# Optimization experiments

Measured on AMD Instinct MI355X. Metric: run time of the kernel, lower is better.

Reference implementation:

```python
import jax, jax.numpy as jnp
import numpy as np

K = 5  # spline kernel size per dim (dim=3 -> 125 kernels)
NS = [20000, 5000, 1280, 320, 80, 32, 16]
ES = [320000, 80000, 20480, 5120, 1280, 512]
NF = [2, 16, 32, 64, 128, 128, 128]

_BITS = jnp.array([[(b >> d) & 1 for d in range(3)] for b in range(8)], dtype=jnp.int32)  # [8,3]
_STRIDES = jnp.array([1, K, K * K], dtype=jnp.int32)


def spline_conv(x, edge_index, pseudo, W, root, bias):
    """SplineConv, dim=3, kernel_size=5, degree-1 open B-splines, mean aggregation.
    x: [N,Cin], edge_index: [2,E], pseudo: [E,3] in [0,1], W: [125,Cin,Cout]."""
    N, Cin = x.shape
    src, dst = edge_index[0], edge_index[1]
    p = pseudo * (K - 1)                                  # [E,3]
    k0 = jnp.clip(jnp.floor(p), 0.0, K - 2)
    frac = p - k0                                         # [E,3]
    k0 = k0.astype(jnp.int32)
    # degree-1 basis: 2^3 = 8 active kernel corners per edge
    w = jnp.where(_BITS[None] == 1, frac[:, None, :], 1.0 - frac[:, None, :])  # [E,8,3]
    wprod = jnp.prod(w, axis=-1)                          # [E,8]
    kidx = jnp.sum((k0[:, None, :] + _BITS[None]) * _STRIDES, axis=-1)         # [E,8]
    xj = x[src]                                           # gather [E,Cin]
    # scatter weighted source features into (dst node, kernel) buckets
    seg = (dst[:, None] * (K ** 3) + kidx).reshape(-1)    # [E*8]
    contrib = (wprod[..., None] * xj[:, None, :]).reshape(-1, Cin)
    A = jax.ops.segment_sum(contrib, seg, num_segments=N * K ** 3).reshape(N, K ** 3, Cin)
    out = jnp.einsum('nki,kio->no', A, W)                 # [N,Cout]
    deg = jax.ops.segment_sum(jnp.ones(src.shape[0], x.dtype), dst, num_segments=N)
    out = out / jnp.maximum(deg, 1.0)[:, None]            # mean aggregation
    return out + x @ root + bias                          # root weight + bias


def _forward(x, eis, eas, Ps, Ws, Rs, bs):
    for l in range(6):
        h = jax.nn.elu(spline_conv(x, eis[l], eas[l], Ws[l], Rs[l], bs[l]))
        x = Ps[l].T @ h                                   # pool to coarser mesh
    return jnp.max(x, axis=0)[None, :]                    # AdaptiveMaxPool1d(1) over nodes -> [1,128]


def setup_inputs() -> dict:
    key = jax.random.key(0)
    ks = iter(jax.random.split(key, 64))
    inp = {"x": jax.random.normal(next(ks), (NS[0], NF[0]), jnp.float32)}
    for l in range(6):
        inp[f"ei{l}"] = jax.random.randint(next(ks), (2, ES[l]), 0, NS[l], dtype=jnp.int32)
        inp[f"ea{l}"] = jax.random.uniform(next(ks), (ES[l], 3), jnp.float32)
    pnames = ["P01", "P12", "P23", "P34", "P45", "P56"]
    for l, pn in enumerate(pnames):
        inp[pn] = jax.random.normal(next(ks), (NS[l], NS[l + 1]), jnp.float32) * (NS[l] ** -0.5)
    for l in range(6):
        cin, cout = NF[l], NF[l + 1]
        inp[f"W{l+1}"] = jax.random.normal(next(ks), (K ** 3, cin, cout), jnp.float32) * 0.05
        inp[f"R{l+1}"] = jax.random.normal(next(ks), (cin, cout), jnp.float32) * (cin ** -0.5)
        inp[f"b{l+1}"] = jnp.zeros((cout,), jnp.float32)
    return inp


def reference(x, ei0, ea0, ei1, ea1, ei2, ea2, ei3, ea3, ei4, ea4, ei5, ea5,
              P01, P12, P23, P34, P45, P56,
              W1, R1, b1, W2, R2, b2, W3, R3, b3,
              W4, R4, b4, W5, R5, b5, W6, R6, b6):
    eis = [ei0, ei1, ei2, ei3, ei4, ei5]
    eas = [ea0, ea1, ea2, ea3, ea4, ea5]
    Ps = [P01, P12, P23, P34, P45, P56]
    Ws = [W1, W2, W3, W4, W5, W6]
    Rs = [R1, R2, R3, R4, R5, R6]
    bs = [b1, b2, b3, b4, b5, b6]
    return _forward(x, eis, eas, Ps, Ws, Rs, bs)
```

## Files before the change

### kernel.cpp

```cpp
#include <hip/hip_runtime.h>
#include <math.h>

#define NKER 125

struct Ptr6i { const int* p[6]; };
struct Ptr6f { const float* p[6]; };

__global__ __launch_bounds__(256) void hist_all_kernel(Ptr6i eis, int* __restrict__ hist) {
  static const int EB[7] = {0, 1250, 1563, 1643, 1663, 1668, 1670};
  static const int Es[6] = {320000, 80000, 20480, 5120, 1280, 512};
  static const int hOff[6] = {0, 20000, 25000, 26280, 26600, 26680};
  int b = blockIdx.x;
  int l = 0;
  while (b >= EB[l + 1]) l++;
  int e = (b - EB[l]) * 256 + threadIdx.x;
  if (e < Es[l]) atomicAdd(&hist[hOff[l] + eis.p[l][Es[l] + e]], 1);
}

__global__ __launch_bounds__(1024) void scan6_kernel(int* __restrict__ hist,
                                                     int* __restrict__ start,
                                                     int* __restrict__ cursor) {
  static const int histOff[6] = {0, 20000, 25000, 26280, 26600, 26680};
  static const int startOff[6] = {0, 20001, 25002, 26283, 26604, 26685};
  static const int Nl[6] = {20000, 5000, 1280, 320, 80, 32};
  __shared__ int ps[1024];
  int b = blockIdx.x;
  int* h = hist + histOff[b];
  int* s = start + startOff[b];
  int* c = cursor + histOff[b];
  int N = Nl[b];
  int t = threadIdx.x;
  int chunk = (N + 1023) / 1024;
  int lo = min(N, t * chunk), hi = min(N, lo + chunk);
  int sum = 0;
  for (int i = lo; i < hi; i++) sum += h[i];
  ps[t] = sum;
  __syncthreads();
  for (int off = 1; off < 1024; off <<= 1) {
    int v = (t >= off) ? ps[t - off] : 0;
    __syncthreads();
    ps[t] += v;
    __syncthreads();
  }
  int base = (t == 0) ? 0 : ps[t - 1];
  for (int i = lo; i < hi; i++) {
    int hv = h[i];
    s[i] = base;
    c[i] = base;
    base += hv;
  }
  if (t == 1023) s[N] = ps[1023];
}

__global__ __launch_bounds__(256) void reorder_all_kernel(
    Ptr6i eis, Ptr6f eas, int* __restrict__ cursor,
    int* __restrict__ srcS, int* __restrict__ kpkS, float* __restrict__ frS) {
  static const int EB[7] = {0, 1250, 1563, 1643, 1663, 1668, 1670};
  static const int Es[6] = {320000, 80000, 20480, 5120, 1280, 512};
  static const int hOff[6] = {0, 20000, 25000, 26280, 26600, 26680};
  static const int EoffK[6] = {0, 320000, 400000, 420480, 425600, 426880};
  int b = blockIdx.x;
  int l = 0;
  while (b >= EB[l + 1]) l++;
  int e = (b - EB[l]) * 256 + threadIdx.x;
  if (e >= Es[l]) return;
  const int* ei = eis.p[l];
  const float* ea = eas.p[l];
  int src = ei[e];
  int dst = ei[Es[l] + e];
  int kpk = 0;
  float f[3];
#pragma unroll
  for (int d = 0; d < 3; d++) {
    float p = ea[e * 3 + d] * 4.0f;
    float kf = fminf(fmaxf(floorf(p), 0.0f), 3.0f);
    f[d] = p - kf;
    kpk |= ((int)kf) << (4 * d);
  }
  int pos = EoffK[l] + atomicAdd(&cursor[hOff[l] + dst], 1);
  srcS[pos] = src;
  kpkS[pos] = kpk;
  frS[pos * 3 + 0] = f[0];
  frS[pos * 3 + 1] = f[1];
  frS[pos * 3 + 2] = f[2];
}

template <int CINSH, int G, int KDIM, int KSG, int NT>
__global__ __launch_bounds__(NT) void build2_kernel(
    const int* __restrict__ start, const int* __restrict__ srcS,
    const int* __restrict__ kpkS, const float* __restrict__ frS,
    const float* __restrict__ x, float* __restrict__ A) {
  __shared__ float rows[G * KDIM];
  const int Cin = 1 << CINSH;
  int tid = threadIdx.x;
  int n0 = blockIdx.x * G;
  for (int t = tid; t < G * KDIM / 4; t += NT)
    ((float4*)rows)[t] = make_float4(0.0f, 0.0f, 0.0f, 0.0f);
  __syncthreads();
  int nl = tid >> CINSH;
  int ci = tid & (Cin - 1);
  int n = n0 + nl;
  int e0 = start[n], e1 = start[n + 1];
  float* row = rows + nl * KDIM + ci;
  for (int e = e0; e < e1; e++) {
    int src = srcS[e];
    int kpk = kpkS[e];
    float f0 = frS[3 * e], f1 = frS[3 * e + 1], f2 = frS[3 * e + 2];
    float xv = x[((size_t)src << CINSH) + ci];
    float g0 = 1.0f - f0, g1 = 1.0f - f1, g2 = 1.0f - f2;
    int kb = (kpk & 15) + 5 * ((kpk >> 4) & 15) + 25 * ((kpk >> 8) & 15);
    float* rb = row + (kb << CINSH);
    rb[0]              += (g0 * g1 * g2) * xv;
    rb[1 << CINSH]     += (f0 * g1 * g2) * xv;
    rb[5 << CINSH]     += (g0 * f1 * g2) * xv;
    rb[6 << CINSH]     += (f0 * f1 * g2) * xv;
    rb[25 << CINSH]    += (g0 * g1 * f2) * xv;
    rb[26 << CINSH]    += (f0 * g1 * f2) * xv;
    rb[30 << CINSH]    += (g0 * f1 * f2) * xv;
    rb[31 << CINSH]    += (f0 * f1 * f2) * xv;
  }
  __syncthreads();
  const int RQ = KSG / 4;
  for (int t = tid; t < G * RQ; t += NT) {
    int r = t / RQ, c4 = t % RQ;
    int c = c4 * 4;
    float4 v = make_float4(0.0f, 0.0f, 0.0f, 0.0f);
    if (c < KDIM) v = *(const float4*)&rows[r * KDIM + c];
    ((float4*)&A[(size_t)(n0 + r) * KSG])[c4] = v;
  }
}

__global__ __launch_bounds__(128) void build2_l0_kernel(
    const int* __restrict__ start, const int* __restrict__ srcS,
    const int* __restrict__ kpkS, const float* __restrict__ frS,
    const float* __restrict__ x, float* __restrict__ A, int N) {
  __shared__ float rows[64 * 254];
  int tid = threadIdx.x;
  int n0 = blockIdx.x * 64;
  for (int t = tid; t < 64 * 254 / 4; t += 128)
    ((float4*)rows)[t] = make_float4(0.0f, 0.0f, 0.0f, 0.0f);
  __syncthreads();
  int nl = tid >> 1;
  int ci = tid & 1;
  int n = n0 + nl;
  if (n < N) {
    int e0 = start[n], e1 = start[n + 1];
    float* row = rows + nl * 254 + ci;
    for (int e = e0; e < e1; e++) {
      int src = srcS[e];
      int kpk = kpkS[e];
      float f0 = frS[3 * e], f1 = frS[3 * e + 1], f2 = frS[3 * e + 2];
      float xv = x[(size_t)src * 2 + ci];
      float g0 = 1.0f - f0, g1 = 1.0f - f1, g2 = 1.0f - f2;
      int kb = (kpk & 15) + 5 * ((kpk >> 4) & 15) + 25 * ((kpk >> 8) & 15);
      float* rb = row + kb * 2;
      rb[0]  = fmaf(g0 * g1 * g2, xv, rb[0]);
      rb[2]  = fmaf(f0 * g1 * g2, xv, rb[2]);
      rb[10] = fmaf(g0 * f1 * g2, xv, rb[10]);
      rb[12] = fmaf(f0 * f1 * g2, xv, rb[12]);
      rb[50] = fmaf(g0 * g1 * f2, xv, rb[50]);
      rb[52] = fmaf(f0 * g1 * f2, xv, rb[52]);
      rb[60] = fmaf(g0 * f1 * f2, xv, rb[60]);
      rb[62] = fmaf(f0 * f1 * f2, xv, rb[62]);
    }
  }
  __syncthreads();
  for (int it = 0; it < 32; it++) {
    int sub = tid >> 6;
    int c4 = tid & 63;
    int nn = n0 + it * 2 + sub;
    if (nn >= N) continue;
    float4 v = make_float4(0.0f, 0.0f, 0.0f, 0.0f);
    if (c4 < 63) v = *(const float4*)&rows[(it * 2 + sub) * 254 + c4 * 4];
    ((float4*)&A[(size_t)nn * 256])[c4] = v;
  }
}

template <int BM, int COUT, int NT>
__global__ __launch_bounds__(NT) void gemm3_kernel(
    const float* __restrict__ A, const float* __restrict__ W,
    float* __restrict__ gpart, int M, int Kdim, int KS, int ktiles) {
  const int BK = 32;
  __shared__ float At[BK][BM + 4];
  __shared__ float Wl[BK][COUT];
  const int TC = COUT / 4;
  int tid = threadIdx.x;
  int tc = tid % TC;
  int tr = tid / TC;
  int m0 = blockIdx.x * BM;
  int kbeg = blockIdx.y * ktiles * BK;
  int kend = min(KS, kbeg + ktiles * BK);
  float ar[4][4];
#pragma unroll
  for (int i = 0; i < 4; i++)
#pragma unroll
    for (int j = 0; j < 4; j++) ar[i][j] = 0.0f;

  for (int k0 = kbeg; k0 < kend; k0 += BK) {
    for (int t = tid; t < BM * (BK / 4); t += NT) {
      int c4 = t % (BK / 4), r = t / (BK / 4);
      int m = m0 + r;
      float4 v = make_float4(0.0f, 0.0f, 0.0f, 0.0f);
      if (m < M) v = *(const float4*)&A[(size_t)m * KS + k0 + c4 * 4];
      At[c4 * 4 + 0][r] = v.x; At[c4 * 4 + 1][r] = v.y;
      At[c4 * 4 + 2][r] = v.z; At[c4 * 4 + 3][r] = v.w;
    }
    int kleft = Kdim - k0;
    if (kleft >= BK) {
      for (int t = tid; t < BK * COUT / 4; t += NT)
        ((float4*)&Wl[0][0])[t] = ((const float4*)&W[(size_t)k0 * COUT])[t];
    } else {
      for (int t = tid; t < BK * COUT; t += NT) {
        int kk = t / COUT, o = t % COUT;
        Wl[kk][o] = (kk < kleft) ? W[(size_t)(k0 + kk) * COUT + o] : 0.0f;
      }
    }
    __syncthreads();
#pragma unroll
    for (int kk = 0; kk < BK; kk++) {
      float4 a = *(const float4*)&At[kk][tr * 4];
      float4 w = *(const float4*)&Wl[kk][tc * 4];
      float av[4] = {a.x, a.y, a.z, a.w};
      float wv[4] = {w.x, w.y, w.z, w.w};
#pragma unroll
      for (int i = 0; i < 4; i++)
#pragma unroll
        for (int j = 0; j < 4; j++)
          ar[i][j] = fmaf(av[i], wv[j], ar[i][j]);
    }
    __syncthreads();
  }
  float* gp = gpart + ((size_t)blockIdx.y * M) * COUT + tc * 4;
#pragma unroll
  for (int i = 0; i < 4; i++) {
    int m = m0 + tr * 4 + i;
    if (m < M)
      *(float4*)(gp + (size_t)m * COUT) =
          make_float4(ar[i][0], ar[i][1], ar[i][2], ar[i][3]);
  }
}

__global__ __launch_bounds__(256) void epilogue_kernel(
    const float* __restrict__ gpart, const int* __restrict__ degI,
    const float* __restrict__ x, const float* __restrict__ R,
    const float* __restrict__ b, float* __restrict__ h,
    int N, int Cin, int coutShift, int kchunks) {
  int tid = blockIdx.x * 256 + threadIdx.x;
  int Cout = 1 << coutShift;
  if (tid >= (N << coutShift)) return;
  int n = tid >> coutShift;
  int o = tid & (Cout - 1);
  size_t stride = (size_t)N << coutShift;
  float s = 0.0f;
  for (int c = 0; c < kchunks; c++) s += gpart[(size_t)c * stride + tid];
  s /= (float)max(degI[n], 1);
  float r = b[o];
  const float* xr = &x[n * Cin];
  for (int i = 0; i < Cin; i++) r = fmaf(xr[i], R[i * Cout + o], r);
  float v = s + r;
  h[tid] = v > 0.0f ? v : expm1f(v);
}

#define FMA4(c, pj, h) \
  c.x = fmaf(pj, h.x, c.x); c.y = fmaf(pj, h.y, c.y); \
  c.z = fmaf(pj, h.z, c.z); c.w = fmaf(pj, h.w, c.w);

template <int COUT, int OPT>
__global__ __launch_bounds__(256) void pool5b_kernel(
    const float* __restrict__ P, const float* __restrict__ h,
    float* __restrict__ partial, int Nsrc, int Nnext, int chunk, int items) {
  extern __shared__ float hs[];
  int c = blockIdx.y;
  int n0 = c * chunk;
  int n1 = min(Nsrc, n0 + chunk);
  int len = n1 - n0;
  for (int t = threadIdx.x; t < len * (COUT / 4); t += 256)
    ((float4*)hs)[t] = ((const float4*)&h[(size_t)n0 * COUT])[t];
  __syncthreads();
  int item = blockIdx.x * 256 + threadIdx.x;
  if (item >= items) return;
  int nj4 = Nnext >> 2;
  int j0 = (item % nj4) << 2;
  int o0 = (item / nj4) * OPT;
  const float4 z = make_float4(0.0f, 0.0f, 0.0f, 0.0f);
  float4 c00 = z, c01 = z, c02 = z, c03 = z;
  float4 c10 = z, c11 = z, c12 = z, c13 = z;
  float4 c20 = z, c21 = z, c22 = z, c23 = z;
  float4 c30 = z, c31 = z, c32 = z, c33 = z;
  const float* Pb = P + j0;

#define USTEP(pv, nn)                                                    \
  {                                                                      \
    const float4* hr = (const float4*)&hs[(nn) * COUT + o0];             \
    float4 h0 = hr[0], h1 = hr[1];                                       \
    FMA4(c00, pv.x, h0) FMA4(c01, pv.x, h1)                              \
    FMA4(c10, pv.y, h0) FMA4(c11, pv.y, h1)                              \
    FMA4(c20, pv.z, h0) FMA4(c21, pv.z, h1)                              \
    FMA4(c30, pv.w, h0) FMA4(c31, pv.w, h1)                              \
    if constexpr (OPT == 16) {                                           \
      float4 h2 = hr[2], h3 = hr[3];                                     \
      FMA4(c02, pv.x, h2) FMA4(c03, pv.x, h3)                            \
      FMA4(c12, pv.y, h2) FMA4(c13, pv.y, h3)                            \
      FMA4(c22, pv.z, h2) FMA4(c23, pv.z, h3)                            \
      FMA4(c32, pv.w, h2) FMA4(c33, pv.w, h3)                            \
    }                                                                    \
  }

  int n = 0;
  for (; n + 4 <= len; n += 4) {
    float4 pv0 = *(const float4*)&Pb[(size_t)(n0 + n + 0) * Nnext];
    float4 pv1 = *(const float4*)&Pb[(size_t)(n0 + n + 1) * Nnext];
    float4 pv2 = *(const float4*)&Pb[(size_t)(n0 + n + 2) * Nnext];
    float4 pv3 = *(const float4*)&Pb[(size_t)(n0 + n + 3) * Nnext];
    USTEP(pv0, n + 0)
    USTEP(pv1, n + 1)
    USTEP(pv2, n + 2)
    USTEP(pv3, n + 3)
  }
  for (; n < len; n++) {
    float4 pv = *(const float4*)&Pb[(size_t)(n0 + n) * Nnext];
    USTEP(pv, n)
  }
#undef USTEP

  float* pp = partial + ((size_t)c * Nnext + j0) * COUT + o0;
  *(float4*)(pp + 0 * COUT + 0) = c00;
  *(float4*)(pp + 0 * COUT + 4) = c01;
  *(float4*)(pp + 1 * COUT + 0) = c10;
  *(float4*)(pp + 1 * COUT + 4) = c11;
  *(float4*)(pp + 2 * COUT + 0) = c20;
  *(float4*)(pp + 2 * COUT + 4) = c21;
  *(float4*)(pp + 3 * COUT + 0) = c30;
  *(float4*)(pp + 3 * COUT + 4) = c31;
  if constexpr (OPT == 16) {
    *(float4*)(pp + 0 * COUT + 8)  = c02;
    *(float4*)(pp + 0 * COUT + 12) = c03;
    *(float4*)(pp + 1 * COUT + 8)  = c12;
    *(float4*)(pp + 1 * COUT + 12) = c13;
    *(float4*)(pp + 2 * COUT + 8)  = c22;
    *(float4*)(pp + 2 * COUT + 12) = c23;
    *(float4*)(pp + 3 * COUT + 8)  = c32;
    *(float4*)(pp + 3 * COUT + 12) = c33;
  }
}

__global__ __launch_bounds__(256) void preduce_kernel(
    const float* __restrict__ partial, float* __restrict__ xnext,
    int NnCout, int chunks) {
  int i = blockIdx.x * 256 + threadIdx.x;
  if (i >= NnCout) return;
  float s = 0.0f;
  for (int c = 0; c < chunks; c++) s += partial[(size_t)c * NnCout + i];
  xnext[i] = s;
}

__global__ __launch_bounds__(128) void max_kernel(const float* __restrict__ x6,
                                                  float* __restrict__ out) {
  int o = threadIdx.x;
  float m = -3.0e38f;
  for (int n = 0; n < 16; n++) m = fmaxf(m, x6[n * 128 + o]);
  out[o] = m;
}

extern "C" void kernel_launch(void* const* d_in, const int* in_sizes, int n_in,
                              void* d_out, int out_size, void* d_ws, size_t ws_size,
                              hipStream_t stream) {
  static const int NSh[7] = {20000, 5000, 1280, 320, 80, 32, 16};
  static const int ESh[6] = {320000, 80000, 20480, 5120, 1280, 512};
  static const int NFh[7] = {2, 16, 32, 64, 128, 128, 128};
  static const int cinSh[6]  = {1, 4, 5, 6, 7, 7};
  static const int coutSh[6] = {4, 5, 6, 7, 7, 7};
  static const int KSt[6] = {256, 2016, 4000, 8000, 16000, 16000};
  static const int kchunksTab[6] = {4, 8, 16, 32, 64, 128};
  static const int ktilesTab[6]  = {2, 8, 8, 8, 8, 4};
  static const int poolChunksTab[6] = {250, 80, 16, 8, 4, 2};
  static const int histOff[6] = {0, 20000, 25000, 26280, 26600, 26680};
  static const int startOff[6] = {0, 20001, 25002, 26283, 26604, 26685};
  static const int Eoff[6] = {0, 320000, 400000, 420480, 425600, 426880};

  const float* x0 = (const float*)d_in[0];
  Ptr6i eis;
  Ptr6f eas;
  for (int l = 0; l < 6; l++) {
    eis.p[l] = (const int*)d_in[1 + 2 * l];
    eas.p[l] = (const float*)d_in[2 + 2 * l];
  }
  const float* Pm[6];
  for (int l = 0; l < 6; l++) Pm[l] = (const float*)d_in[13 + l];
  const float* Wt[6];
  const float* Rt[6];
  const float* bt[6];
  for (int l = 0; l < 6; l++) {
    Wt[l] = (const float*)d_in[19 + 3 * l];
    Rt[l] = (const float*)d_in[20 + 3 * l];
    bt[l] = (const float*)d_in[21 + 3 * l];
  }

  float* ws = (float*)d_ws;
  float* A     = ws;
  float* gpart = ws + 10150000;
  float* hbuf  = ws + 11500000;
  float* ppart = ws + 12000000;
  float* xA    = ws + 32100000;
  float* xB    = ws + 32200000;
  int* hist    = (int*)(ws + 32300000);
  int* startA  = (int*)(ws + 32330000);
  int* cursor  = (int*)(ws + 32360000);
  int* srcS    = (int*)(ws + 32390000);
  int* kpkS    = (int*)(ws + 32900000);
  float* frS   = ws + 33400000;

  hipMemsetAsync(hist, 0, 26712 * sizeof(int), stream);
  hist_all_kernel<<<1670, 256, 0, stream>>>(eis, hist);
  scan6_kernel<<<6, 1024, 0, stream>>>(hist, startA, cursor);
  reorder_all_kernel<<<1670, 256, 0, stream>>>(eis, eas, cursor, srcS, kpkS, frS);

  const float* cur = x0;
  for (int l = 0; l < 6; l++) {
    int N = NSh[l], Nn = NSh[l + 1], Cin = NFh[l], Cout = NFh[l + 1];
    int Kdim = NKER * Cin, KS = KSt[l];
    float* xnext = (l & 1) ? xB : xA;
    const int* st = startA + startOff[l];
    const int* ss = srcS + Eoff[l];
    const int* kk = kpkS + Eoff[l];
    const float* ff = frS + 3 * (size_t)Eoff[l];

    switch (l) {
      case 0: build2_l0_kernel<<<313, 128, 0, stream>>>(st, ss, kk, ff, cur, A, N); break;
      case 1: build2_kernel<4, 8, 2000, 2016, 128><<<625, 128, 0, stream>>>(st, ss, kk, ff, cur, A); break;
      case 2: build2_kernel<5, 4, 4000, 4000, 128><<<320, 128, 0, stream>>>(st, ss, kk, ff, cur, A); break;
      case 3: build2_kernel<6, 2, 8000, 8000, 128><<<160, 128, 0, stream>>>(st, ss, kk, ff, cur, A); break;
      case 4: build2_kernel<7, 1, 16000, 16000, 128><<<80, 128, 0, stream>>>(st, ss, kk, ff, cur, A); break;
      default: build2_kernel<7, 1, 16000, 16000, 128><<<32, 128, 0, stream>>>(st, ss, kk, ff, cur, A); break;
    }

    int kchunks = kchunksTab[l], ktiles = ktilesTab[l];
    switch (l) {
      case 0: {
        dim3 g((N + 127) / 128, kchunks);
        gemm3_kernel<128, 16, 128><<<g, 128, 0, stream>>>(A, Wt[l], gpart, N, Kdim, KS, ktiles);
        break;
      }
      case 1: {
        dim3 g((N + 127) / 128, kchunks);
        gemm3_kernel<128, 32, 256><<<g, 256, 0, stream>>>(A, Wt[l], gpart, N, Kdim, KS, ktiles);
        break;
      }
      case 2: {
        dim3 g((N + 63) / 64, kchunks);
        gemm3_kernel<64, 64, 256><<<g, 256, 0, stream>>>(A, Wt[l], gpart, N, Kdim, KS, ktiles);
        break;
      }
      default: {
        dim3 g((N + 31) / 32, kchunks);
        gemm3_kernel<32, 128, 256><<<g, 256, 0, stream>>>(A, Wt[l], gpart, N, Kdim, KS, ktiles);
        break;
      }
    }

    int ethreads = N << coutSh[l];
    epilogue_kernel<<<(ethreads + 255) / 256, 256, 0, stream>>>(
        gpart, hist + histOff[l], cur, Rt[l], bt[l], hbuf, N, Cin, coutSh[l], kchunks);

    int pc = poolChunksTab[l];
    int chunk = (N + pc - 1) / pc;
    size_t ldsB = (size_t)chunk * Cout * sizeof(float);
    int items, gx;
    switch (Cout) {
      case 16:
        items = (Nn >> 2) * 1;
        gx = (items + 255) / 256;
        pool5b_kernel<16, 16><<<dim3(gx, pc), 256, ldsB, stream>>>(Pm[l], hbuf, ppart, N, Nn, chunk, items);
        break;
      case 32:
        items = (Nn >> 2) * 2;
        gx = (items + 255) / 256;
        pool5b_kernel<32, 16><<<dim3(gx, pc), 256, ldsB, stream>>>(Pm[l], hbuf, ppart, N, Nn, chunk, items);
        break;
      case 64:
        items = (Nn >> 2) * 8;
        gx = (items + 255) / 256;
        pool5b_kernel<64, 8><<<dim3(gx, pc), 256, ldsB, stream>>>(Pm[l], hbuf, ppart, N, Nn, chunk, items);
        break;
      default:
        items = (Nn >> 2) * 16;
        gx = (items + 255) / 256;
        pool5b_kernel<128, 8><<<dim3(gx, pc), 256, ldsB, stream>>>(Pm[l], hbuf, ppart, N, Nn, chunk, items);
        break;
    }
    int NnCout = Nn << coutSh[l];
    preduce_kernel<<<(NnCout + 255) / 256, 256, 0, stream>>>(ppart, xnext, NnCout, pc);

    cur = xnext;
  }

  max_kernel<<<1, 128, 0, stream>>>(cur, (float*)d_out);
}
```

Measured before the change: 823.4 us.

## Pack sorted edge records into float4 and precompute atomic ranks during histogram

The histogram pass now records each edge's atomic rank within its destination bucket, so the placement pass computes its position from the scanned start offsets instead of doing a second round of atomics on a cursor array. Each sorted edge is stored as one float4 record, with src and the packed kernel index bit-packed into the first word and the three fractions in the rest. This lets the build kernels fetch an edge with one 16-byte load instead of five scalar loads. The pooling chunk count for layer 0 is also lowered. The bit packing relies on src fitting in 15 bits, which holds for node counts up to 32768.

Measured after the change: 755.1 us. -8.3%, faster.

```diff
diff --git a/kernel.cpp b/kernel.cpp
--- a/kernel.cpp
+++ b/kernel.cpp
@@ -6,28 +6,31 @@
 struct Ptr6i { const int* p[6]; };
 struct Ptr6f { const float* p[6]; };
 
-__global__ __launch_bounds__(256) void hist_all_kernel(Ptr6i eis, int* __restrict__ hist) {
+__global__ __launch_bounds__(256) void rank_all_kernel(Ptr6i eis, int* __restrict__ cnt,
+                                                       int* __restrict__ rankS) {
   static const int EB[7] = {0, 1250, 1563, 1643, 1663, 1668, 1670};
   static const int Es[6] = {320000, 80000, 20480, 5120, 1280, 512};
   static const int hOff[6] = {0, 20000, 25000, 26280, 26600, 26680};
+  static const int EoffK[6] = {0, 320000, 400000, 420480, 425600, 426880};
   int b = blockIdx.x;
   int l = 0;
   while (b >= EB[l + 1]) l++;
   int e = (b - EB[l]) * 256 + threadIdx.x;
-  if (e < Es[l]) atomicAdd(&hist[hOff[l] + eis.p[l][Es[l] + e]], 1);
-}
-
-__global__ __launch_bounds__(1024) void scan6_kernel(int* __restrict__ hist,
-                                                     int* __restrict__ start,
-                                                     int* __restrict__ cursor) {
+  if (e >= Es[l]) return;
+  int dst = eis.p[l][Es[l] + e];
+  int r = atomicAdd(&cnt[hOff[l] + dst], 1);
+  rankS[EoffK[l] + e] = r;
+}
+
+__global__ __launch_bounds__(1024) void scan6_kernel(const int* __restrict__ hist,
+                                                     int* __restrict__ start) {
   static const int histOff[6] = {0, 20000, 25000, 26280, 26600, 26680};
   static const int startOff[6] = {0, 20001, 25002, 26283, 26604, 26685};
   static const int Nl[6] = {20000, 5000, 1280, 320, 80, 32};
   __shared__ int ps[1024];
   int b = blockIdx.x;
-  int* h = hist + histOff[b];
+  const int* h = hist + histOff[b];
   int* s = start + startOff[b];
-  int* c = cursor + histOff[b];
   int N = Nl[b];
   int t = threadIdx.x;
   int chunk = (N + 1023) / 1024;
@@ -44,20 +47,18 @@
   }
   int base = (t == 0) ? 0 : ps[t - 1];
   for (int i = lo; i < hi; i++) {
-    int hv = h[i];
     s[i] = base;
-    c[i] = base;
-    base += hv;
+    base += h[i];
   }
   if (t == 1023) s[N] = ps[1023];
 }
 
-__global__ __launch_bounds__(256) void reorder_all_kernel(
-    Ptr6i eis, Ptr6f eas, int* __restrict__ cursor,
-    int* __restrict__ srcS, int* __restrict__ kpkS, float* __restrict__ frS) {
+__global__ __launch_bounds__(256) void place_all_kernel(
+    Ptr6i eis, Ptr6f eas, const int* __restrict__ startA,
+    const int* __restrict__ rankS, float4* __restrict__ recS) {
   static const int EB[7] = {0, 1250, 1563, 1643, 1663, 1668, 1670};
   static const int Es[6] = {320000, 80000, 20480, 5120, 1280, 512};
-  static const int hOff[6] = {0, 20000, 25000, 26280, 26600, 26680};
+  static const int sOff[6] = {0, 20001, 25002, 26283, 26604, 26685};
   static const int EoffK[6] = {0, 320000, 400000, 420480, 425600, 426880};
   int b = blockIdx.x;
   int l = 0;
@@ -77,18 +78,14 @@
     f[d] = p - kf;
     kpk |= ((int)kf) << (4 * d);
   }
-  int pos = EoffK[l] + atomicAdd(&cursor[hOff[l] + dst], 1);
-  srcS[pos] = src;
-  kpkS[pos] = kpk;
-  frS[pos * 3 + 0] = f[0];
-  frS[pos * 3 + 1] = f[1];
-  frS[pos * 3 + 2] = f[2];
+  int pos = startA[sOff[l] + dst] + rankS[EoffK[l] + e];
+  recS[EoffK[l] + pos] =
+      make_float4(__uint_as_float((unsigned)src | ((unsigned)kpk << 15)), f[0], f[1], f[2]);
 }
 
 template <int CINSH, int G, int KDIM, int KSG, int NT>
-__global__ __launch_bounds__(NT) void build2_kernel(
-    const int* __restrict__ start, const int* __restrict__ srcS,
-    const int* __restrict__ kpkS, const float* __restrict__ frS,
+__global__ __launch_bounds__(NT) void build3_kernel(
+    const int* __restrict__ start, const float4* __restrict__ recS,
     const float* __restrict__ x, float* __restrict__ A) {
   __shared__ float rows[G * KDIM];
   const int Cin = 1 << CINSH;
@@ -103,9 +100,11 @@
   int e0 = start[n], e1 = start[n + 1];
   float* row = rows + nl * KDIM + ci;
   for (int e = e0; e < e1; e++) {
-    int src = srcS[e];
-    int kpk = kpkS[e];
-    float f0 = frS[3 * e], f1 = frS[3 * e + 1], f2 = frS[3 * e + 2];
+    float4 rec = recS[e];
+    unsigned v = __float_as_uint(rec.x);
+    int src = v & 0x7fff;
+    int kpk = v >> 15;
+    float f0 = rec.y, f1 = rec.z, f2 = rec.w;
     float xv = x[((size_t)src << CINSH) + ci];
     float g0 = 1.0f - f0, g1 = 1.0f - f1, g2 = 1.0f - f2;
     int kb = (kpk & 15) + 5 * ((kpk >> 4) & 15) + 25 * ((kpk >> 8) & 15);
@@ -130,9 +129,8 @@
   }
 }
 
-__global__ __launch_bounds__(128) void build2_l0_kernel(
-    const int* __restrict__ start, const int* __restrict__ srcS,
-    const int* __restrict__ kpkS, const float* __restrict__ frS,
+__global__ __launch_bounds__(128) void build3_l0_kernel(
+    const int* __restrict__ start, const float4* __restrict__ recS,
     const float* __restrict__ x, float* __restrict__ A, int N) {
   __shared__ float rows[64 * 254];
   int tid = threadIdx.x;
@@ -147,9 +145,11 @@
     int e0 = start[n], e1 = start[n + 1];
     float* row = rows + nl * 254 + ci;
     for (int e = e0; e < e1; e++) {
-      int src = srcS[e];
-      int kpk = kpkS[e];
-      float f0 = frS[3 * e], f1 = frS[3 * e + 1], f2 = frS[3 * e + 2];
+      float4 rec = recS[e];
+      unsigned v = __float_as_uint(rec.x);
+      int src = v & 0x7fff;
+      int kpk = v >> 15;
+      float f0 = rec.y, f1 = rec.z, f2 = rec.w;
       float xv = x[(size_t)src * 2 + ci];
       float g0 = 1.0f - f0, g1 = 1.0f - f1, g2 = 1.0f - f2;
       int kb = (kpk & 15) + 5 * ((kpk >> 4) & 15) + 25 * ((kpk >> 8) & 15);
@@ -366,14 +366,13 @@
                               void* d_out, int out_size, void* d_ws, size_t ws_size,
                               hipStream_t stream) {
   static const int NSh[7] = {20000, 5000, 1280, 320, 80, 32, 16};
-  static const int ESh[6] = {320000, 80000, 20480, 5120, 1280, 512};
   static const int NFh[7] = {2, 16, 32, 64, 128, 128, 128};
   static const int cinSh[6]  = {1, 4, 5, 6, 7, 7};
   static const int coutSh[6] = {4, 5, 6, 7, 7, 7};
   static const int KSt[6] = {256, 2016, 4000, 8000, 16000, 16000};
   static const int kchunksTab[6] = {4, 8, 16, 32, 64, 128};
   static const int ktilesTab[6]  = {2, 8, 8, 8, 8, 4};
-  static const int poolChunksTab[6] = {250, 80, 16, 8, 4, 2};
+  static const int poolChunksTab[6] = {120, 80, 16, 8, 4, 2};
   static const int histOff[6] = {0, 20000, 25000, 26280, 26600, 26680};
   static const int startOff[6] = {0, 20001, 25002, 26283, 26604, 26685};
   static const int Eoff[6] = {0, 320000, 400000, 420480, 425600, 426880};
@@ -405,15 +404,13 @@
   float* xB    = ws + 32200000;
   int* hist    = (int*)(ws + 32300000);
   int* startA  = (int*)(ws + 32330000);
-  int* cursor  = (int*)(ws + 32360000);
-  int* srcS    = (int*)(ws + 32390000);
-  int* kpkS    = (int*)(ws + 32900000);
-  float* frS   = ws + 33400000;
+  int* rankS   = (int*)(ws + 32390000);
+  float4* recS = (float4*)(ws + 33000000);
 
   hipMemsetAsync(hist, 0, 26712 * sizeof(int), stream);
-  hist_all_kernel<<<1670, 256, 0, stream>>>(eis, hist);
-  scan6_kernel<<<6, 1024, 0, stream>>>(hist, startA, cursor);
-  reorder_all_kernel<<<1670, 256, 0, stream>>>(eis, eas, cursor, srcS, kpkS, frS);
+  rank_all_kernel<<<1670, 256, 0, stream>>>(eis, hist, rankS);
+  scan6_kernel<<<6, 1024, 0, stream>>>(hist, startA);
+  place_all_kernel<<<1670, 256, 0, stream>>>(eis, eas, startA, rankS, recS);
 
   const float* cur = x0;
   for (int l = 0; l < 6; l++) {
@@ -421,17 +418,15 @@
     int Kdim = NKER * Cin, KS = KSt[l];
     float* xnext = (l & 1) ? xB : xA;
     const int* st = startA + startOff[l];
-    const int* ss = srcS + Eoff[l];
-    const int* kk = kpkS + Eoff[l];
-    const float* ff = frS + 3 * (size_t)Eoff[l];
+    const float4* rc = recS + Eoff[l];
 
     switch (l) {
-      case 0: build2_l0_kernel<<<313, 128, 0, stream>>>(st, ss, kk, ff, cur, A, N); break;
-      case 1: build2_kernel<4, 8, 2000, 2016, 128><<<625, 128, 0, stream>>>(st, ss, kk, ff, cur, A); break;
-      case 2: build2_kernel<5, 4, 4000, 4000, 128><<<320, 128, 0, stream>>>(st, ss, kk, ff, cur, A); break;
-      case 3: build2_kernel<6, 2, 8000, 8000, 128><<<160, 128, 0, stream>>>(st, ss, kk, ff, cur, A); break;
-      case 4: build2_kernel<7, 1, 16000, 16000, 128><<<80, 128, 0, stream>>>(st, ss, kk, ff, cur, A); break;
-      default: build2_kernel<7, 1, 16000, 16000, 128><<<32, 128, 0, stream>>>(st, ss, kk, ff, cur, A); break;
+      case 0: build3_l0_kernel<<<313, 128, 0, stream>>>(st, rc, cur, A, N); break;
+      case 1: build3_kernel<4, 8, 2000, 2016, 128><<<625, 128, 0, stream>>>(st, rc, cur, A); break;
+      case 2: build3_kernel<5, 4, 4000, 4000, 128><<<320, 128, 0, stream>>>(st, rc, cur, A); break;
+      case 3: build3_kernel<6, 2, 8000, 8000, 128><<<160, 128, 0, stream>>>(st, rc, cur, A); break;
+      case 4: build3_kernel<7, 1, 16000, 16000, 128><<<80, 128, 0, stream>>>(st, rc, cur, A); break;
+      default: build3_kernel<7, 1, 16000, 16000, 128><<<32, 128, 0, stream>>>(st, rc, cur, A); break;
     }
 
     int kchunks = kchunksTab[l], ktiles = ktilesTab[l];
```
